# Performance work log

Hardware: AMD Instinct MI355X
Metric: run time of the kernel (lower is better)

The kernel has to match this reference:

```python
import jax, jax.numpy as jnp
import numpy as np

NUM_CLASSES = 80
TOP_K = 200
CONF_T = 0.05
NMS_T = 0.5
CROP = 300.0
A = 49104
B = 8
NEG = -1.0  # dead-score sentinel; real scores are sigmoid outputs in (0,1)


def setup_inputs() -> dict:
    key = jax.random.key(0)
    k1, k2, k3, k4, k5, k6 = jax.random.split(key, 6)
    # structured, plausible anchors in (ymin, xmin, ymax, xmax), pixel coords
    yc = jax.random.uniform(k1, (A,)) * CROP
    xc = jax.random.uniform(k2, (A,)) * CROP
    h = 10.0 + jax.random.uniform(k5, (A,)) * 90.0
    w = 10.0 + jax.random.uniform(k6, (A,)) * 90.0
    anchors = jnp.stack([yc - h / 2, xc - w / 2, yc + h / 2, xc + w / 2], axis=-1)
    confidences = jax.random.normal(k3, (B, A, NUM_CLASSES + 1), dtype=jnp.float32)
    regressions = jax.random.normal(k4, (B, A, 4), dtype=jnp.float32) * 0.1
    return {"confidences": confidences, "regressions": regressions, "anchors": anchors}


def _decode(regressions, anchors):
    yca = (anchors[:, 0] + anchors[:, 2]) / 2
    xca = (anchors[:, 1] + anchors[:, 3]) / 2
    ha = anchors[:, 2] - anchors[:, 0]
    wa = anchors[:, 3] - anchors[:, 1]
    w = jnp.exp(regressions[..., 3]) * wa
    h = jnp.exp(regressions[..., 2]) * ha
    yc = regressions[..., 0] * ha + yca
    xc = regressions[..., 1] * wa + xca
    # clamp exactly as the original: min-clamp on xmin/ymin, max-clamp on xmax/ymax
    xmin = jnp.maximum(xc - w / 2, 0.0) / CROP
    ymin = jnp.maximum(yc - h / 2, 0.0) / CROP
    xmax = jnp.minimum(xc + w / 2, CROP - 1.0) / CROP
    ymax = jnp.minimum(yc + h / 2, CROP - 1.0) / CROP
    return jnp.stack([xmin, ymin, xmax, ymax], axis=-1)  # [B,A,4] (x1,y1,x2,y2)


def _iou_one_to_many(box, boxes):
    x1 = jnp.maximum(box[0], boxes[:, 0])
    y1 = jnp.maximum(box[1], boxes[:, 1])
    x2 = jnp.minimum(box[2], boxes[:, 2])
    y2 = jnp.minimum(box[3], boxes[:, 3])
    inter = jnp.maximum(x2 - x1, 0.0) * jnp.maximum(y2 - y1, 0.0)
    area_b = (box[2] - box[0]) * (box[3] - box[1])
    areas = (boxes[:, 2] - boxes[:, 0]) * (boxes[:, 3] - boxes[:, 1])
    union = area_b + areas - inter
    return jnp.where(union > 0, inter / union, 0.0)


def _nms_image(boxes, probs):
    # boxes: [A,4], probs: [A,C] (sigmoid, background stripped)
    scores = jnp.max(probs, axis=1)
    classes = jnp.argmax(probs, axis=1)
    valid = scores > CONF_T
    # batched_nms trick: offset boxes per class so cross-class IoU is 0
    offset = classes.astype(boxes.dtype) * (jnp.max(boxes) + 1.0)
    boxes_o = boxes + offset[:, None]
    live = jnp.where(valid, scores, NEG)

    def body(live, _):
        idx = jnp.argmax(live)
        keep = live[idx] > 0.0
        iou = _iou_one_to_many(boxes_o[idx], boxes_o)
        live = jnp.where(keep & (iou > NMS_T), NEG, live)
        live = live.at[idx].set(NEG)
        return live, (idx, keep)

    _, (idxs, keeps) = jax.lax.scan(body, live, None, length=TOP_K)
    cls_k = classes[idxs]          # [TOP_K]
    sc_k = scores[idxs]            # [TOP_K]
    bx_k = boxes[idxs]             # [TOP_K,4]
    # per-class slot = rank among kept detections of the same class (keep order is score-descending)
    onehot = (cls_k[:, None] == jnp.arange(NUM_CLASSES)[None, :]) & keeps[:, None]
    slot = jnp.cumsum(onehot, axis=0)[jnp.arange(TOP_K), cls_k] - 1
    rows = jnp.where(keeps, cls_k + 1, NUM_CLASSES + 1)  # OOB row when dropped
    slot = jnp.where(keeps, slot, TOP_K)                 # OOB col when dropped
    vals = jnp.concatenate([sc_k[:, None], bx_k], axis=1)  # [TOP_K,5]
    out = jnp.zeros((NUM_CLASSES + 1, TOP_K, 5), boxes.dtype)
    return out.at[rows, slot].set(vals, mode="drop")


def reference(confidences, regressions, anchors):
    probs = jax.nn.sigmoid(confidences[:, :, 1:])
    boxes = _decode(regressions, anchors)
    return jax.vmap(_nms_image)(boxes, probs)  # [B, C+1, TOP_K, 5]
```

## Files before the change

kernel.cpp:

```cpp
#include <hip/hip_runtime.h>
#include <stdint.h>

#define NCLS 80
#define TOPK 200
#define CONF_T 0.05f
#define CONF_BITS 0x3D4CCCCDu
#define CROPF 300.0f
#define NA 49104
#define NB 8
#define NSEL 256
#define MKEYS 4096
#define APB 64
#define T1 256
#define CHUNK (APB * 81)
#define NGRP (NA / 16)
#define MROW 5
#define OUTFLO ((NCLS + 1) * TOPK * 5)
#define NBLK1 ((NB * NA) / APB)
#define BASE13 125542u
#define NBINS 4512
#define RUNL 71

__device__ __forceinline__ void decode_box(const float4 rg, const float4 an,
                                           float& x1, float& y1, float& x2, float& y2) {
    float yca = (an.x + an.z) * 0.5f;
    float xca = (an.y + an.w) * 0.5f;
    float ha = an.z - an.x;
    float wa = an.w - an.y;
    float w = expf(rg.w) * wa;
    float h = expf(rg.z) * ha;
    float yc = rg.x * ha + yca;
    float xc = rg.y * wa + xca;
    x1 = fmaxf(xc - w * 0.5f, 0.0f) / CROPF;
    y1 = fmaxf(yc - h * 0.5f, 0.0f) / CROPF;
    x2 = fminf(xc + w * 0.5f, CROPF - 1.0f) / CROPF;
    y2 = fminf(yc + h * 0.5f, CROPF - 1.0f) / CROPF;
}

__device__ __forceinline__ float rlf(float v, int l) {
    return __int_as_float(__builtin_amdgcn_readlane(__float_as_int(v), l));
}

__global__ __launch_bounds__(T1) void phase1_kernel(
    const float* __restrict__ conf, const float* __restrict__ reg,
    const float* __restrict__ anch, unsigned long long* __restrict__ key64,
    float4* __restrict__ boxes, float2* __restrict__ gm2,
    float* __restrict__ outz)
{
    __shared__ float lds[CHUNK];
    const int blk = blockIdx.x, t = threadIdx.x;

    {
        const int gid = blk * T1 + t;
        constexpr int TOT4 = NB * OUTFLO / 4;
        if (gid < TOT4)
            reinterpret_cast<float4*>(outz)[gid] = make_float4(0.f, 0.f, 0.f, 0.f);
    }

    const float4* src = reinterpret_cast<const float4*>(conf + (size_t)blk * CHUNK);
    float4* dst = reinterpret_cast<float4*>(lds);
    for (int i = t; i < CHUNK / 4; i += T1) dst[i] = src[i];
    __syncthreads();

    const int la = t >> 2, sub = t & 3;
    const int quad = blk * APB + la;
    const float* crow = lds + la * 81;
    float best = -3.0e38f; int bc = 255;
    #pragma unroll
    for (int k = 0; k < 20; ++k) {
        int c = 1 + sub + 4 * k;
        float v = crow[c];
        if (v > best) { best = v; bc = c; }
    }
    for (int m = 1; m <= 2; m <<= 1) {
        float ov = __shfl_xor(best, m);
        int oc = __shfl_xor(bc, m);
        if (ov > best || (ov == best && oc < bc)) { best = ov; bc = oc; }
    }
    unsigned long long key = 0ull;
    float bmaxl = 0.0f;
    if (sub == 0) {
        int a = quad % NA;
        float s = 1.0f / (1.0f + expf(-best));
        uint32_t ginv = 0x1FFFFu - (uint32_t)a;
        key = ((unsigned long long)__float_as_uint(s) << 32)
            | (unsigned long long)((ginv << 7) | (uint32_t)(bc - 1));
        float4 rg = reinterpret_cast<const float4*>(reg)[quad];
        float4 an = reinterpret_cast<const float4*>(anch)[a];
        float x1, y1, x2, y2; decode_box(rg, an, x1, y1, x2, y2);
        boxes[quad] = make_float4(x1, y1, x2, y2);
        bmaxl = fmaxf(fmaxf(x1, y1), fmaxf(x2, y2));
    }
    {
        const int lane = t & 63, w = t >> 6;
        unsigned long long kk = __shfl(key, (lane & 15) * 4);
        if (lane < 16)
            key64[(size_t)blk * APB + w * 16 + lane] = kk;
    }
    float wbest = best;
    #pragma unroll
    for (int m = 1; m < 64; m <<= 1) {
        wbest = fmaxf(wbest, __shfl_xor(wbest, m));
        bmaxl = fmaxf(bmaxl, __shfl_xor(bmaxl, m));
    }
    if ((t & 63) == 0)
        gm2[blk * 4 + (t >> 6)] = make_float2(1.0f / (1.0f + expf(-wbest)), bmaxl);
}

__global__ __launch_bounds__(1024) void phase2_kernel(
    const unsigned long long* __restrict__ key64, const float4* __restrict__ boxes,
    const float2* __restrict__ gm2, float* __restrict__ out)
{
    __shared__ uint64_t s_keys[MKEYS];
    __shared__ uint64_t s_skeys[MKEYS];
    __shared__ float    s_gm[NGRP + 3];
    __shared__ uint64_t s_mask[256 * MROW];
    __shared__ float4   s_boxo[256];
    __shared__ float4   s_braw[256];
    __shared__ float    s_areao[256];
    __shared__ float4   s_keptbox[TOPK];
    __shared__ uint64_t s_clsmask[NCLS][4];
    __shared__ uint32_t s_ccount[NCLS];
    __shared__ uint32_t s_shv[8];
    __shared__ float    s_bmaxarr[16];
    __shared__ float    s_offm;
    __shared__ uint8_t  s_clsl[256];
    __shared__ uint64_t s_K[4];

    uint32_t* hist = (uint32_t*)s_keys;

    const int b = blockIdx.x;
    const int t = threadIdx.x;

    for (int i = t; i < NBINS; i += 1024) hist[i] = 0;
    if (t < NCLS * 4) ((uint64_t*)s_clsmask)[t] = 0ull;
    if (t < 8) s_shv[t] = 0;
    __syncthreads();

    {
        const float2* gmb = gm2 + (size_t)b * NGRP;
        float wm = 0.0f;
        for (int i = t; i < NGRP; i += 1024) {
            float2 v = gmb[i];
            s_gm[i] = v.x;
            wm = fmaxf(wm, v.y);
            if (v.x > CONF_T) {
                int ib = (int)((__float_as_uint(v.x) >> 13) - BASE13);
                ib = max(0, min(NBINS - 1, ib));
                atomicAdd(&hist[ib], 1u);
            }
        }
        #pragma unroll
        for (int m = 1; m < 64; m <<= 1) wm = fmaxf(wm, __shfl_xor(wm, m));
        if ((t & 63) == 0) s_bmaxarr[t >> 6] = wm;
    }
    __syncthreads();

    if (t < 64) {
        const int lane = t;
        uint32_t run = 0;
        const int base = lane * RUNL;
        #pragma unroll
        for (int k = 0; k < RUNL; ++k) {
            int ib = base + k;
            run += (ib < NBINS) ? hist[ib] : 0u;
        }
        uint32_t S = run;
        #pragma unroll
        for (int m = 1; m < 64; m <<= 1) {
            uint32_t o = __shfl_down(S, m);
            if (lane + m < 64) S += o;
        }
        uint64_t bal = __ballot(S >= NSEL);
        int L = bal ? (63 - __builtin_clzll(bal)) : -1;
        uint32_t SnextL = (L >= 0 && L < 63)
            ? (uint32_t)__builtin_amdgcn_readlane((int)S, L + 1) : 0u;
        if (lane == 0) {
            uint32_t t13 = 0;
            if (L >= 0) {
                uint32_t running = SnextL;
                for (int k = RUNL - 1; k >= 0; --k) {
                    int ib = L * RUNL + k;
                    if (ib >= NBINS) continue;
                    running += hist[ib];
                    if (running >= NSEL) { t13 = BASE13 + (uint32_t)ib; break; }
                }
            }
            s_shv[3] = t13;
        }
    } else if (t < 128) {
        const int lane2 = t - 64;
        float m = (lane2 < 16) ? s_bmaxarr[lane2] : 0.0f;
        #pragma unroll
        for (int s = 1; s < 64; s <<= 1) m = fmaxf(m, __shfl_xor(m, s));
        if (lane2 == 0) s_offm = m + 1.0f;
    }
    __syncthreads();

    const uint32_t T13 = s_shv[3];
    for (int i = t; i < NGRP; i += 1024) {
        float s = s_gm[i];
        if (s > CONF_T && (__float_as_uint(s) >> 13) >= T13) {
            const unsigned long long* kp = key64 + (size_t)b * NA + (size_t)i * 16;
            #pragma unroll
            for (int j = 0; j < 16; ++j) {
                unsigned long long key = kp[j];
                uint32_t bits = (uint32_t)(key >> 32);
                if (bits > CONF_BITS && (bits >> 13) >= T13) {
                    uint32_t p = atomicAdd(&s_shv[4], 1u);
                    if (p < MKEYS) s_keys[p] = key;
                }
            }
        }
    }
    __syncthreads();
    uint32_t nGa = s_shv[4]; if (nGa > MKEYS) nGa = MKEYS;
    const int lim = (nGa < 256u) ? (int)nGa : 256;

    {
        const int lane = t & 63;
        const uint32_t nch = (nGa + 63) >> 6;
        for (int s = 0; s < MKEYS / 1024; ++s) {
            int kid = t + s * 1024;
            bool act = kid < (int)nGa;
            if (__ballot(act) == 0ull) continue;
            uint64_t my = act ? s_keys[kid] : ~0ull;
            uint32_t r = 0;
            for (uint32_t ch = 0; ch < nch; ++ch) {
                uint32_t src = ch * 64 + (uint32_t)lane;
                uint64_t kc = (src < nGa) ? s_keys[src] : 0ull;
                uint32_t clo = (uint32_t)kc, chi = (uint32_t)(kc >> 32);
                for (int jj = 0; jj < 64; ++jj) {
                    uint32_t olo = (uint32_t)__builtin_amdgcn_readlane((int)clo, jj);
                    uint32_t ohi = (uint32_t)__builtin_amdgcn_readlane((int)chi, jj);
                    uint64_t ok = ((uint64_t)ohi << 32) | olo;
                    r += (ok > my) ? 1u : 0u;
                }
            }
            if (act) s_skeys[r] = my;
        }
    }
    __syncthreads();

    const float offm = s_offm;
    if (t < 256) {
        if (t < lim) {
            uint64_t key = s_skeys[t];
            uint32_t low = (uint32_t)key;
            int c = (int)(low & 0x7Fu);
            uint32_t g = 0x1FFFFu - (low >> 7);
            s_clsl[t] = (uint8_t)c;
            float4 br = boxes[(size_t)b * NA + g];
            s_braw[t] = br;
            float off = (float)c * offm;
            float4 bo = make_float4(br.x + off, br.y + off, br.z + off, br.w + off);
            s_boxo[t] = bo;
            s_areao[t] = (bo.z - bo.x) * (bo.w - bo.y);
        } else {
            s_clsl[t] = 0;
            s_braw[t] = make_float4(0.f, 0.f, 0.f, 0.f);
            s_boxo[t] = make_float4(0.f, 0.f, 0.f, 0.f);
            s_areao[t] = 0.f;
        }
    }
    __syncthreads();

    {
        const int wv = t >> 6, lane = t & 63;
        const int rbase = (wv & 3) * 64, c = wv >> 2;
        const int i = rbase + lane;
        float4 bi = s_boxo[i];
        float aI = s_areao[i];
        float4 vj = s_boxo[c * 64 + lane];
        float vA = s_areao[c * 64 + lane];
        uint64_t m = 0ull;
        for (int jj = 0; jj < 64; ++jj) {
            float bx1 = rlf(vj.x, jj), by1 = rlf(vj.y, jj);
            float bx2 = rlf(vj.z, jj), by2 = rlf(vj.w, jj);
            float aJ  = rlf(vA, jj);
            float ix1 = fmaxf(bi.x, bx1), iy1 = fmaxf(bi.y, by1);
            float ix2 = fminf(bi.z, bx2), iy2 = fminf(bi.w, by2);
            float inter = fmaxf(ix2 - ix1, 0.f) * fmaxf(iy2 - iy1, 0.f);
            float uni = aI + aJ - inter;
            if (uni > 0.f && inter + inter > uni) m |= (1ull << jj);
        }
        s_mask[(size_t)i * MROW + c] = m;
    }
    __syncthreads();

    if (t < 64) {
        const int lane = t;
        uint64_t mr[4][4];
        #pragma unroll
        for (int wr = 0; wr < 4; ++wr)
            #pragma unroll
            for (int wc = 0; wc < 4; ++wc)
                mr[wr][wc] = s_mask[(size_t)(wr * 64 + lane) * MROW + wc];
        const uint64_t below = (lane == 0) ? 0ull : ((~0ull) >> (64 - lane));
        uint64_t K[4];
        #pragma unroll
        for (int w = 0; w < 4; ++w) {
            int lo = w * 64, n = lim - lo;
            K[w] = (n >= 64) ? ~0ull : (n > 0 ? ((~0ull) >> (64 - n)) : 0ull);
        }
        for (int round = 0; round < 257; ++round) {
            uint64_t nK[4];
            #pragma unroll
            for (int wr = 0; wr < 4; ++wr) {
                uint64_t dead = 0ull;
                #pragma unroll
                for (int w = 0; w < 4; ++w) {
                    uint64_t mm = mr[wr][w] & K[w];
                    if (w < wr) dead |= mm;
                    else if (w == wr) dead |= (mm & below);
                }
                bool nb = (dead == 0ull) && (wr * 64 + lane < lim);
                nK[wr] = __ballot(nb);
            }
            bool same = (nK[0] == K[0]) && (nK[1] == K[1]) &&
                        (nK[2] == K[2]) && (nK[3] == K[3]);
            K[0] = nK[0]; K[1] = nK[1]; K[2] = nK[2]; K[3] = nK[3];
            if (same) break;
        }
        if (lane < 4) s_K[lane] = K[lane];
    }
    __syncthreads();

    if (t < 256 && ((s_K[(t >> 6) & 3] >> (t & 63)) & 1ull))
        atomicOr(&s_clsmask[s_clsl[t]][(t >> 6) & 3], 1ull << (t & 63));
    __syncthreads();

    {
        const int jw = (t >> 6) & 3, jb = t & 63;
        bool kept = (t < 256) && ((s_K[jw] >> jb) & 1ull);
        if (kept) {
            const uint64_t below = (jb == 0) ? 0ull : ((~0ull) >> (64 - jb));
            uint32_t ord = (uint32_t)__popcll(s_K[jw] & below);
            for (int w = 0; w < jw; ++w) ord += (uint32_t)__popcll(s_K[w]);
            if (ord < TOPK) {
                int c = (int)s_clsl[t];
                const uint64_t* cm = s_clsmask[c];
                uint32_t slot = (uint32_t)__popcll(cm[jw] & below);
                for (int w = 0; w < jw; ++w) slot += (uint32_t)__popcll(cm[w]);
                float scv = __uint_as_float((uint32_t)(s_skeys[t] >> 32));
                float4 br = s_braw[t];
                float* o = out + (((size_t)b * (NCLS + 1) + (size_t)(c + 1)) * TOPK + slot) * 5;
                o[0] = scv; o[1] = br.x; o[2] = br.y; o[3] = br.z; o[4] = br.w;
                s_keptbox[ord] = s_boxo[t];
            }
        }
    }
    __syncthreads();

    if (t == 0) {
        uint32_t nk = 0;
        #pragma unroll
        for (int w = 0; w < 4; ++w) nk += (uint32_t)__popcll(s_K[w]);
        if (nk < TOPK && nGa > (uint32_t)lim) {
            for (int c = 0; c < NCLS; ++c) {
                uint32_t n = 0;
                #pragma unroll
                for (int w = 0; w < 4; ++w) n += (uint32_t)__popcll(s_clsmask[c][w]);
                s_ccount[c] = n;
            }
            for (uint32_t ci = (uint32_t)lim; ci < nGa && nk < TOPK; ++ci) {
                uint64_t key = s_skeys[ci];
                uint32_t low = (uint32_t)key;
                int c = (int)(low & 0x7Fu);
                uint32_t g = 0x1FFFFu - (low >> 7);
                float4 br = boxes[(size_t)b * NA + g];
                float off = (float)c * offm;
                float4 bo = make_float4(br.x + off, br.y + off, br.z + off, br.w + off);
                float aB2 = (bo.z - bo.x) * (bo.w - bo.y);
                bool sup = false;
                for (uint32_t k2 = 0; k2 < nk && !sup; ++k2) {
                    float4 kb = s_keptbox[k2];
                    float aK = (kb.z - kb.x) * (kb.w - kb.y);
                    float ix1 = fmaxf(bo.x, kb.x), iy1 = fmaxf(bo.y, kb.y);
                    float ix2 = fminf(bo.z, kb.z), iy2 = fminf(bo.w, kb.w);
                    float inter = fmaxf(ix2 - ix1, 0.f) * fmaxf(iy2 - iy1, 0.f);
                    float uni = aB2 + aK - inter;
                    sup = (uni > 0.f && inter + inter > uni);
                }
                if (!sup) {
                    uint32_t slot = s_ccount[c]; s_ccount[c] = slot + 1;
                    float scv = __uint_as_float((uint32_t)(key >> 32));
                    float* o = out + (((size_t)b * (NCLS + 1) + (size_t)(c + 1)) * TOPK + slot) * 5;
                    o[0] = scv; o[1] = br.x; o[2] = br.y; o[3] = br.z; o[4] = br.w;
                    s_keptbox[nk] = bo;
                    ++nk;
                }
            }
        }
    }
}

extern "C" void kernel_launch(void* const* d_in, const int* in_sizes, int n_in,
                              void* d_out, int out_size, void* d_ws, size_t ws_size,
                              hipStream_t stream)
{
    const float* conf = (const float*)d_in[0];
    const float* reg  = (const float*)d_in[1];
    const float* anch = (const float*)d_in[2];
    float* out = (float*)d_out;

    char* ws = (char*)d_ws;
    unsigned long long* key64 = (unsigned long long*)ws;
    float4* boxes = (float4*)(ws + (size_t)NB * NA * 8);
    float2* gm2 = (float2*)(ws + (size_t)NB * NA * 24);

    phase1_kernel<<<NBLK1, T1, 0, stream>>>(conf, reg, anch, key64, boxes, gm2, out);
    phase2_kernel<<<NB, 1024, 0, stream>>>(key64, boxes, gm2, out);
}
```

Baseline: 71.34 us.

## Speculatively collect high-score candidates in phase1 to skip phase2 histogram selection

Phase1 now appends every anchor whose best score is at least a fixed threshold of 0.975 into per-image, per-subgroup candidate lists, using wave-aggregated atomics. Phase2 checks whether the combined count lies between NSEL and MKEYS with no subgroup overflowing. If so, it copies those keys straight into shared memory and skips the histogram build, the threshold search and the key64 rescan. Otherwise it falls back to the old path, which now batches its atomics per group. This adds a memset launch and extra global writes in phase1, and depends on the score distribution to hit the fast path.

```diff
diff --git a/kernel.cpp b/kernel.cpp
--- a/kernel.cpp
+++ b/kernel.cpp
@@ -5,6 +5,7 @@
 #define TOPK 200
 #define CONF_T 0.05f
 #define CONF_BITS 0x3D4CCCCDu
+#define T0F 0.975f
 #define CROPF 300.0f
 #define NA 49104
 #define NB 8
@@ -20,6 +21,8 @@
 #define BASE13 125542u
 #define NBINS 4512
 #define RUNL 71
+#define NSUB 64
+#define SUBCAP 64
 
 __device__ __forceinline__ void decode_box(const float4 rg, const float4 an,
                                            float& x1, float& y1, float& x2, float& y2) {
@@ -45,6 +48,7 @@
     const float* __restrict__ conf, const float* __restrict__ reg,
     const float* __restrict__ anch, unsigned long long* __restrict__ key64,
     float4* __restrict__ boxes, float2* __restrict__ gm2,
+    uint32_t* __restrict__ subcnt, unsigned long long* __restrict__ speclist,
     float* __restrict__ outz)
 {
     __shared__ float lds[CHUNK];
@@ -78,12 +82,12 @@
         if (ov > best || (ov == best && oc < bc)) { best = ov; bc = oc; }
     }
     unsigned long long key = 0ull;
-    float bmaxl = 0.0f;
+    float bmaxl = 0.0f, sflt = -1.0f;
     if (sub == 0) {
         int a = quad % NA;
-        float s = 1.0f / (1.0f + expf(-best));
+        sflt = 1.0f / (1.0f + expf(-best));
         uint32_t ginv = 0x1FFFFu - (uint32_t)a;
-        key = ((unsigned long long)__float_as_uint(s) << 32)
+        key = ((unsigned long long)__float_as_uint(sflt) << 32)
             | (unsigned long long)((ginv << 7) | (uint32_t)(bc - 1));
         float4 rg = reinterpret_cast<const float4*>(reg)[quad];
         float4 an = reinterpret_cast<const float4*>(anch)[a];
@@ -97,6 +101,27 @@
         if (lane < 16)
             key64[(size_t)blk * APB + w * 16 + lane] = kk;
     }
+    {
+        const int lane = t & 63, w = t >> 6;
+        bool qual = (sub == 0) && (sflt >= T0F);
+        uint64_t bal = __ballot(qual);
+        if (bal) {
+            int grp_g = blk * 4 + w;
+            int bimg = grp_g / NGRP;
+            int subl = (grp_g % NGRP) & (NSUB - 1);
+            int leader = __builtin_ctzll(bal);
+            uint32_t n = (uint32_t)__popcll(bal);
+            uint32_t base = 0;
+            if (lane == leader)
+                base = atomicAdd(&subcnt[bimg * NSUB + subl], n);
+            base = (uint32_t)__shfl((int)base, leader);
+            if (qual) {
+                uint32_t pos = base + (uint32_t)__popcll(bal & ((1ull << lane) - 1ull));
+                if (pos < SUBCAP)
+                    speclist[(size_t)bimg * MKEYS + (size_t)subl * SUBCAP + pos] = key;
+            }
+        }
+    }
     float wbest = best;
     #pragma unroll
     for (int m = 1; m < 64; m <<= 1) {
@@ -109,7 +134,8 @@
 
 __global__ __launch_bounds__(1024) void phase2_kernel(
     const unsigned long long* __restrict__ key64, const float4* __restrict__ boxes,
-    const float2* __restrict__ gm2, float* __restrict__ out)
+    const float2* __restrict__ gm2, const uint32_t* __restrict__ subcnt,
+    const unsigned long long* __restrict__ speclist, float* __restrict__ out)
 {
     __shared__ uint64_t s_keys[MKEYS];
     __shared__ uint64_t s_skeys[MKEYS];
@@ -121,6 +147,7 @@
     __shared__ float4   s_keptbox[TOPK];
     __shared__ uint64_t s_clsmask[NCLS][4];
     __shared__ uint32_t s_ccount[NCLS];
+    __shared__ uint32_t s_cnt[NSUB], s_off[NSUB];
     __shared__ uint32_t s_shv[8];
     __shared__ float    s_bmaxarr[16];
     __shared__ float    s_offm;
@@ -132,7 +159,6 @@
     const int b = blockIdx.x;
     const int t = threadIdx.x;
 
-    for (int i = t; i < NBINS; i += 1024) hist[i] = 0;
     if (t < NCLS * 4) ((uint64_t*)s_clsmask)[t] = 0ull;
     if (t < 8) s_shv[t] = 0;
     __syncthreads();
@@ -144,76 +170,114 @@
             float2 v = gmb[i];
             s_gm[i] = v.x;
             wm = fmaxf(wm, v.y);
-            if (v.x > CONF_T) {
-                int ib = (int)((__float_as_uint(v.x) >> 13) - BASE13);
+        }
+        #pragma unroll
+        for (int m = 1; m < 64; m <<= 1) wm = fmaxf(wm, __shfl_xor(wm, m));
+        if ((t & 63) == 0) s_bmaxarr[t >> 6] = wm;
+    }
+    if (t < NSUB) {
+        uint32_t c = subcnt[b * NSUB + t];
+        uint64_t bad = __ballot(c > SUBCAP);
+        uint32_t x = c;
+        #pragma unroll
+        for (int m = 1; m < 64; m <<= 1) {
+            uint32_t o = __shfl_up(x, m);
+            if (t >= m) x += o;
+        }
+        uint32_t total = (uint32_t)__shfl((int)x, 63);
+        s_cnt[t] = c;
+        s_off[t] = x - c;
+        if (t == 0) {
+            bool fast = (bad == 0ull) && total >= NSEL && total <= MKEYS;
+            s_shv[5] = fast ? 1u : 0u;
+            if (fast) s_shv[4] = total;
+        }
+    }
+    __syncthreads();
+    if (t == 0) {
+        float mx = s_bmaxarr[0];
+        #pragma unroll
+        for (int k = 1; k < 16; ++k) mx = fmaxf(mx, s_bmaxarr[k]);
+        s_offm = mx + 1.0f;
+    }
+
+    const bool fastp = (s_shv[5] != 0);
+    if (fastp) {
+        for (int i = t; i < MKEYS; i += 1024) {
+            int li = i >> 6, idx = i & (SUBCAP - 1);
+            if ((uint32_t)idx < s_cnt[li])
+                s_keys[s_off[li] + idx] = speclist[(size_t)b * MKEYS + i];
+        }
+        __syncthreads();
+    } else {
+        for (int i = t; i < NBINS; i += 1024) hist[i] = 0;
+        __syncthreads();
+        for (int i = t; i < NGRP; i += 1024) {
+            float s = s_gm[i];
+            if (s > CONF_T) {
+                int ib = (int)((__float_as_uint(s) >> 13) - BASE13);
                 ib = max(0, min(NBINS - 1, ib));
                 atomicAdd(&hist[ib], 1u);
             }
         }
-        #pragma unroll
-        for (int m = 1; m < 64; m <<= 1) wm = fmaxf(wm, __shfl_xor(wm, m));
-        if ((t & 63) == 0) s_bmaxarr[t >> 6] = wm;
-    }
-    __syncthreads();
-
-    if (t < 64) {
-        const int lane = t;
-        uint32_t run = 0;
-        const int base = lane * RUNL;
-        #pragma unroll
-        for (int k = 0; k < RUNL; ++k) {
-            int ib = base + k;
-            run += (ib < NBINS) ? hist[ib] : 0u;
-        }
-        uint32_t S = run;
-        #pragma unroll
-        for (int m = 1; m < 64; m <<= 1) {
-            uint32_t o = __shfl_down(S, m);
-            if (lane + m < 64) S += o;
-        }
-        uint64_t bal = __ballot(S >= NSEL);
-        int L = bal ? (63 - __builtin_clzll(bal)) : -1;
-        uint32_t SnextL = (L >= 0 && L < 63)
-            ? (uint32_t)__builtin_amdgcn_readlane((int)S, L + 1) : 0u;
-        if (lane == 0) {
-            uint32_t t13 = 0;
-            if (L >= 0) {
-                uint32_t running = SnextL;
-                for (int k = RUNL - 1; k >= 0; --k) {
-                    int ib = L * RUNL + k;
-                    if (ib >= NBINS) continue;
-                    running += hist[ib];
-                    if (running >= NSEL) { t13 = BASE13 + (uint32_t)ib; break; }
-                }
-            }
-            s_shv[3] = t13;
-        }
-    } else if (t < 128) {
-        const int lane2 = t - 64;
-        float m = (lane2 < 16) ? s_bmaxarr[lane2] : 0.0f;
-        #pragma unroll
-        for (int s = 1; s < 64; s <<= 1) m = fmaxf(m, __shfl_xor(m, s));
-        if (lane2 == 0) s_offm = m + 1.0f;
-    }
-    __syncthreads();
-
-    const uint32_t T13 = s_shv[3];
-    for (int i = t; i < NGRP; i += 1024) {
-        float s = s_gm[i];
-        if (s > CONF_T && (__float_as_uint(s) >> 13) >= T13) {
-            const unsigned long long* kp = key64 + (size_t)b * NA + (size_t)i * 16;
+        __syncthreads();
+        if (t < 64) {
+            const int lane = t;
+            uint32_t run = 0;
+            const int base = lane * RUNL;
             #pragma unroll
-            for (int j = 0; j < 16; ++j) {
-                unsigned long long key = kp[j];
-                uint32_t bits = (uint32_t)(key >> 32);
-                if (bits > CONF_BITS && (bits >> 13) >= T13) {
-                    uint32_t p = atomicAdd(&s_shv[4], 1u);
-                    if (p < MKEYS) s_keys[p] = key;
-                }
-            }
-        }
-    }
-    __syncthreads();
+            for (int k = 0; k < RUNL; ++k) {
+                int ib = base + k;
+                run += (ib < NBINS) ? hist[ib] : 0u;
+            }
+            uint32_t S = run;
+            #pragma unroll
+            for (int m = 1; m < 64; m <<= 1) {
+                uint32_t o = __shfl_down(S, m);
+                if (lane + m < 64) S += o;
+            }
+            uint64_t bal = __ballot(S >= NSEL);
+            int L = bal ? (63 - __builtin_clzll(bal)) : -1;
+            uint32_t SnextL = (L >= 0 && L < 63)
+                ? (uint32_t)__builtin_amdgcn_readlane((int)S, L + 1) : 0u;
+            if (lane == 0) {
+                uint32_t t13 = 0;
+                if (L >= 0) {
+                    uint32_t running = SnextL;
+                    for (int k = RUNL - 1; k >= 0; --k) {
+                        int ib = L * RUNL + k;
+                        if (ib >= NBINS) continue;
+                        running += hist[ib];
+                        if (running >= NSEL) { t13 = BASE13 + (uint32_t)ib; break; }
+                    }
+                }
+                s_shv[3] = t13;
+                s_shv[4] = 0;
+            }
+        }
+        __syncthreads();
+        const uint32_t T13 = s_shv[3];
+        for (int i = t; i < NGRP; i += 1024) {
+            float s = s_gm[i];
+            if (s > CONF_T && (__float_as_uint(s) >> 13) >= T13) {
+                const unsigned long long* kp = key64 + (size_t)b * NA + (size_t)i * 16;
+                unsigned long long kq[16]; uint32_t qm = 0, n = 0;
+                #pragma unroll
+                for (int j = 0; j < 16; ++j) {
+                    kq[j] = kp[j];
+                    uint32_t bits = (uint32_t)(kq[j] >> 32);
+                    if (bits > CONF_BITS && (bits >> 13) >= T13) { qm |= 1u << j; ++n; }
+                }
+                if (n) {
+                    uint32_t p = atomicAdd(&s_shv[4], n);
+                    #pragma unroll
+                    for (int j = 0; j < 16; ++j)
+                        if ((qm >> j) & 1u) { if (p < MKEYS) s_keys[p] = kq[j]; ++p; }
+                }
+            }
+        }
+        __syncthreads();
+    }
     uint32_t nGa = s_shv[4]; if (nGa > MKEYS) nGa = MKEYS;
     const int lim = (nGa < 256u) ? (int)nGa : 256;
 
@@ -408,7 +472,13 @@
     unsigned long long* key64 = (unsigned long long*)ws;
     float4* boxes = (float4*)(ws + (size_t)NB * NA * 8);
     float2* gm2 = (float2*)(ws + (size_t)NB * NA * 24);
-
-    phase1_kernel<<<NBLK1, T1, 0, stream>>>(conf, reg, anch, key64, boxes, gm2, out);
-    phase2_kernel<<<NB, 1024, 0, stream>>>(key64, boxes, gm2, out);
+    char* p = ws + (size_t)NB * NA * 24 + (size_t)NB * NGRP * 8;
+    uint32_t* subcnt = (uint32_t*)p;
+    unsigned long long* speclist =
+        (unsigned long long*)(p + 4096);
+
+    hipMemsetAsync(subcnt, 0, NB * NSUB * sizeof(uint32_t), stream);
+    phase1_kernel<<<NBLK1, T1, 0, stream>>>(conf, reg, anch, key64, boxes, gm2,
+                                            subcnt, speclist, out);
+    phase2_kernel<<<NB, 1024, 0, stream>>>(key64, boxes, gm2, subcnt, speclist, out);
 }
```

Result: slower. 80.57 us (+12.9%).
